# Performance work log

Hardware: AMD Instinct MI355X
Metric: run time of the kernel (lower is better)

Reference implementation:

```python
import jax, jax.numpy as jnp
import numpy as np

N_NODES = 50000
N_EDGES = 800000
IN_DIM = 256
HID_DIM = 128
N_LAYERS = 3


def setup_inputs() -> dict:
    key = jax.random.key(0)
    ks = jax.random.split(key, 7)
    s = 0.05
    x = jax.random.normal(ks[0], (N_NODES, IN_DIM), dtype=jnp.float32)
    edge_index = jax.random.randint(ks[1], (2, N_EDGES), 0, N_NODES, dtype=jnp.int64)
    W_enc = jax.random.normal(ks[2], (HID_DIM, IN_DIM), dtype=jnp.float32) * s
    b_enc = jax.random.normal(ks[3], (HID_DIM,), dtype=jnp.float32) * s
    W_l = jax.random.normal(ks[4], (N_LAYERS, HID_DIM, HID_DIM), dtype=jnp.float32) * s
    b_l = jax.random.normal(ks[5], (N_LAYERS, HID_DIM), dtype=jnp.float32) * s
    W_r = jax.random.normal(ks[6], (N_LAYERS, HID_DIM, HID_DIM), dtype=jnp.float32) * s
    return {"x": x, "edge_index": edge_index, "W_enc": W_enc, "b_enc": b_enc,
            "W_l": W_l, "b_l": b_l, "W_r": W_r}


def reference(x, edge_index, W_enc, b_enc, W_l, b_l, W_r):
    # eval mode: dropout is identity
    n = x.shape[0]
    src, dst = edge_index[0], edge_index[1]
    # encode: Linear(in_dim -> hid_dim)
    h = x @ W_enc.T + b_enc  # [N, H]
    # in-degree for mean aggregation (nodes with no in-edges -> 0 output)
    deg = jax.ops.segment_sum(jnp.ones((src.shape[0],), h.dtype), dst, num_segments=n)
    denom = jnp.maximum(deg, 1.0)[:, None]  # [N, 1]
    for i in range(W_l.shape[0]):
        # mean of source-node features over incoming edges
        agg = jax.ops.segment_sum(h[src], dst, num_segments=n) / denom  # [N, H]
        # SAGEConv: lin_l(agg) + lin_r(h)  (lin_r has no bias)
        h = agg @ W_l[i].T + b_l[i] + h @ W_r[i].T
    return h
```

## Files before the change

### kernel.cpp

```cpp
#include <hip/hip_runtime.h>

#define N_NODES 50000
#define N_EDGES 800000
#define IN_DIM 256
#define HID_DIM 128
#define ROWTILES 3125
#define ENC_BLOCKS 1024
#define WCVT_BLOCKS 48
#define CNT_BLOCKS 256
#define EDGES_PER_CB 3125
#define NBLK_LAYER 1563
#define CAP_E 352
#define TPAD 3136

typedef float f4 __attribute__((ext_vector_type(4)));
typedef float f32x4 __attribute__((ext_vector_type(4)));
typedef float vf2 __attribute__((ext_vector_type(2)));
typedef short bf16x8 __attribute__((ext_vector_type(8)));

__device__ __forceinline__ unsigned short f2bf(float f) {
    unsigned u = __builtin_bit_cast(unsigned, f);
    return (unsigned short)((u + 0x7fffu + ((u >> 16) & 1u)) >> 16);
}
__device__ __forceinline__ unsigned pk2(float a, float b) {
    return (unsigned)f2bf(a) | ((unsigned)f2bf(b) << 16);
}
__device__ __forceinline__ bf16x8 cvt8(f4 a, f4 b) {
    union { bf16x8 v; unsigned u[4]; } r;
    r.u[0] = pk2(a[0], a[1]);
    r.u[1] = pk2(a[2], a[3]);
    r.u[2] = pk2(b[0], b[1]);
    r.u[3] = pk2(b[2], b[3]);
    return r.v;
}
__device__ __forceinline__ vf2 dec8(unsigned short t) {
    return __builtin_amdgcn_cvt_pk_f32_fp8((int)(unsigned)t, false);
}
__device__ __forceinline__ void gl_lds16(const void* g, void* l) {
    __builtin_amdgcn_global_load_lds(
        (const __attribute__((address_space(1))) unsigned int*)g,
        (__attribute__((address_space(3))) unsigned int*)l, 16, 0, 0);
}


__global__ __launch_bounds__(256) void k_pre(const int* __restrict__ dst,
                                             int* __restrict__ Cm,
                                             const float* __restrict__ Wl, const float* __restrict__ Wr,
                                             unsigned short* __restrict__ wlrbf,
                                             const float* __restrict__ x,
                                             const float* __restrict__ Wenc,
                                             const float* __restrict__ bias,
                                             unsigned short* __restrict__ hout,
                                             unsigned char* __restrict__ f8out) {
    __shared__ int smem_i[8192];
    int tid = threadIdx.x;
    if (blockIdx.x < WCVT_BLOCKS) {
        int idx = blockIdx.x * 2048 + tid * 8;
        const float* srcp = (idx < 49152) ? (Wl + idx) : (Wr + (idx - 49152));
        const f4* g = (const f4*)srcp;
        *(bf16x8*)(wlrbf + idx) = cvt8(g[0], g[1]);
        return;
    }
    if (blockIdx.x >= WCVT_BLOCKS + ENC_BLOCKS) {
        int c = blockIdx.x - WCVT_BLOCKS - ENC_BLOCKS;
        int* cnt = smem_i;
        for (int i = tid; i < TPAD; i += 256) cnt[i] = 0;
        __syncthreads();
        const int* dp = dst + c * EDGES_PER_CB;
        for (int i = tid; i < EDGES_PER_CB; i += 256)
            atomicAdd(&cnt[dp[i] >> 4], 1);
        __syncthreads();
        int* crow = Cm + (size_t)c * TPAD;
        for (int t = tid; t < TPAD; t += 256) crow[t] = cnt[t];
        return;
    }
    float* xsf = (float*)smem_i;
    int bid = blockIdx.x - WCVT_BLOCKS;
    int lane = tid & 63;
    int wv = tid >> 6;
    int colbase = wv * 32;
    int lr = lane & 15;
    int kh = (lane >> 4) * 8;
    int khB = kh * 4;
    int swz = (lr & 7) << 4;

    bf16x8 bfr[2][8];
#pragma unroll
    for (int n = 0; n < 2; ++n) {
        const float* wp = Wenc + (size_t)(colbase + n * 16 + lr) * IN_DIM + kh;
#pragma unroll
        for (int s = 0; s < 8; ++s) {
            const f4* g = (const f4*)(wp + s * 32);
            bfr[n][s] = cvt8(g[0], g[1]);
        }
    }
    float bias0 = bias[colbase + lr];
    float bias1 = bias[colbase + 16 + lr];

    int pb = 0;
    for (int rt = bid; rt < ROWTILES; rt += ENC_BLOCKS, pb ^= 1) {
#pragma unroll
        for (int jj = 0; jj < 4; ++jj) {
            int j = wv * 4 + jj;
            const char* gsrc = (const char*)(x + (size_t)(rt * 16 + j) * IN_DIM)
                               + ((lane * 16) ^ ((j & 7) << 4));
            gl_lds16(gsrc, (char*)(xsf + pb * 4096) + j * 1024);
        }
        __syncthreads();

        const char* xb = (const char*)(xsf + pb * 4096) + lr * 1024;
        bf16x8 afr[8];
#pragma unroll
        for (int s = 0; s < 8; ++s) {
            int lo = khB + s * 128;
            f4 a = *(const f4*)(xb + ((lo) ^ swz));
            f4 b = *(const f4*)(xb + ((lo + 16) ^ swz));
            afr[s] = cvt8(a, b);
        }
        f32x4 acc0 = {0.f, 0.f, 0.f, 0.f}, acc1 = {0.f, 0.f, 0.f, 0.f};
#pragma unroll
        for (int s = 0; s < 8; ++s) {
            acc0 = __builtin_amdgcn_mfma_f32_16x16x32_bf16(afr[s], bfr[0][s], acc0, 0, 0, 0);
            acc1 = __builtin_amdgcn_mfma_f32_16x16x32_bf16(afr[s], bfr[1][s], acc1, 0, 0, 0);
        }
        int rbase = rt * 16 + (lane >> 4) * 4;
#pragma unroll
        for (int r = 0; r < 4; ++r) {
            float v0 = acc0[r] + bias0, v1 = acc1[r] + bias1;
            unsigned short* op = hout + (size_t)(rbase + r) * HID_DIM;
            op[colbase + lr] = f2bf(v0);
            op[colbase + 16 + lr] = f2bf(v1);
            unsigned pk = (unsigned)__builtin_amdgcn_cvt_pk_fp8_f32(v0, v1, 0, false);
            unsigned char* fp = f8out + (size_t)(rbase + r) * HID_DIM;
            fp[colbase + lr] = (unsigned char)(pk & 0xff);
            fp[colbase + 16 + lr] = (unsigned char)((pk >> 8) & 0xff);
        }
    }
}


__global__ __launch_bounds__(256) void k_prefix(const int* __restrict__ Cm,
                                                int* __restrict__ STm,
                                                int* __restrict__ tcnt16) {
    int tid = threadIdx.x;
    int lane = tid & 63;
    int t = blockIdx.x * 4 + (tid >> 6);
    if (t >= ROWTILES) return;
    int b0 = lane * 4;
    int c0 = Cm[(size_t)(b0 + 0) * TPAD + t];
    int c1 = Cm[(size_t)(b0 + 1) * TPAD + t];
    int c2 = Cm[(size_t)(b0 + 2) * TPAD + t];
    int c3 = Cm[(size_t)(b0 + 3) * TPAD + t];
    int ls = c0 + c1 + c2 + c3;
    int incl = ls;
#pragma unroll
    for (int off = 1; off < 64; off <<= 1) {
        int v = __shfl_up(incl, off);
        if (lane >= off) incl += v;
    }
    int excl = incl - ls;
    STm[(size_t)(b0 + 0) * TPAD + t] = excl;
    STm[(size_t)(b0 + 1) * TPAD + t] = excl + c0;
    STm[(size_t)(b0 + 2) * TPAD + t] = excl + c0 + c1;
    STm[(size_t)(b0 + 3) * TPAD + t] = excl + c0 + c1 + c2;
    if (lane == 63) tcnt16[t * 16] = incl;
}


__global__ __launch_bounds__(256) void k_scat(const int* __restrict__ src, const int* __restrict__ dst,
                                              const int* __restrict__ STm,
                                              unsigned* __restrict__ buf) {
    __shared__ int sbase[TPAD];
    __shared__ int lcnt[TPAD];
    int tid = threadIdx.x;
    int c = blockIdx.x;
    const int* strow = STm + (size_t)c * TPAD;
    for (int i = tid; i < TPAD; i += 256) { sbase[i] = strow[i]; lcnt[i] = 0; }
    __syncthreads();
    const int* sp = src + c * EDGES_PER_CB;
    const int* dp = dst + c * EDGES_PER_CB;
    for (int i = tid; i < EDGES_PER_CB; i += 256) {
        int sv = sp[i], dv = dp[i];
        int t = dv >> 4, dl = dv & 15;
        int r = atomicAdd(&lcnt[t], 1);
        int slot = sbase[t] + r;
        if (slot < CAP_E) buf[(size_t)t * CAP_E + slot] = (unsigned)sv | ((unsigned)dl << 16);
    }
}


__global__ __launch_bounds__(256) void k_sort2(const unsigned* __restrict__ buf,
                                               const int* __restrict__ tcnt16,
                                               unsigned short* __restrict__ idg,
                                               unsigned short* __restrict__ preft) {
    __shared__ unsigned short stmp[4][512];
    __shared__ int hcur[4][32];
    int tid = threadIdx.x, lane = tid & 63, w = tid >> 6;
    int t = blockIdx.x * 4 + w;
    bool act = t < ROWTILES;
    int cnt = 0;
    if (act) { cnt = tcnt16[t * 16]; if (cnt > CAP_E) cnt = CAP_E; }
    if (lane < 32) hcur[w][lane] = 0;
    unsigned ev[6];
#pragma unroll
    for (int k = 0; k < 6; ++k) {
        int i = lane + k * 64;
        ev[k] = (act && i < cnt) ? buf[(size_t)t * CAP_E + i] : 0xFFFFFFFFu;
    }
    __syncthreads();
#pragma unroll
    for (int k = 0; k < 6; ++k)
        if (ev[k] != 0xFFFFFFFFu) atomicAdd(&hcur[w][ev[k] >> 16], 1);
    __syncthreads();
    int hv = (lane < 16) ? hcur[w][lane] : 0;
    int incl = hv;
#pragma unroll
    for (int off = 1; off <= 16; off <<= 1) {
        int v = __shfl_up(incl, off);
        if (lane >= off) incl += v;
    }
    int excl = incl - hv;
    if (act && lane < 16) hcur[w][16 + lane] = excl;
    if (act && lane <= 16) preft[(size_t)t * 32 + lane] = (unsigned short)excl;
    __syncthreads();
#pragma unroll
    for (int k = 0; k < 6; ++k)
        if (ev[k] != 0xFFFFFFFFu) {
            int r = atomicAdd(&hcur[w][16 + (ev[k] >> 16)], 1);
            stmp[w][r] = (unsigned short)(ev[k] & 0xffff);
        }
    __syncthreads();
    if (act) {
        unsigned* op = (unsigned*)(idg + (size_t)t * 512);
        const unsigned* ip = (const unsigned*)stmp[w];
        int nu = (cnt + 1) >> 1;
        for (int i = lane; i < nu; i += 64) op[i] = ip[i];
    }
}


template <bool LAST>
__global__ __launch_bounds__(256) void k_layer(const unsigned short* __restrict__ H,
                                               const unsigned char* __restrict__ F8,
                                               const unsigned short* __restrict__ idg,
                                               const unsigned short* __restrict__ preft,
                                               const unsigned short* __restrict__ wlbf,
                                               const unsigned short* __restrict__ wrbf,
                                               const float* __restrict__ bias,
                                               unsigned short* __restrict__ hout,
                                               unsigned char* __restrict__ f8out,
                                               float* __restrict__ fout) {
    __shared__ unsigned char rowbuf[CAP_E * 128];
    __shared__ unsigned short aggs[16][136];
    __shared__ unsigned short idsb[2][512];
    int tid = threadIdx.x;
    int lane = tid & 63;
    int wv = tid >> 6;
    int colbase = wv * 32;
    int lr = lane & 15;
    int kh = (lane >> 4) * 8;

    bf16x8 bl[2][4], br[2][4];
#pragma unroll
    for (int n = 0; n < 2; ++n) {
        const unsigned short* lp = wlbf + (size_t)(colbase + n * 16 + lr) * HID_DIM + kh;
        const unsigned short* rp = wrbf + (size_t)(colbase + n * 16 + lr) * HID_DIM + kh;
#pragma unroll
        for (int s = 0; s < 4; ++s) {
            bl[n][s] = *(const bf16x8*)(lp + s * 32);
            br[n][s] = *(const bf16x8*)(rp + s * 32);
        }
    }
    float bias0 = bias[colbase + lr];
    float bias1 = bias[colbase + 16 + lr];

    int rt0 = blockIdx.x;
    gl_lds16((const char*)(idg + (size_t)rt0 * 512) + lane * 16, (void*)idsb[0]);
    int pc = (int)preft[(size_t)rt0 * 32 + (lane < 16 ? lane : 16)];
    asm volatile("s_waitcnt vmcnt(0)" ::: "memory");
    __builtin_amdgcn_sched_barrier(0);

    int pb = 0;
    for (int rt = rt0; rt < ROWTILES; rt += NBLK_LAYER, pb ^= 1) {
        int cnt = __shfl(pc, 16);
        int rb0 = __shfl(pc, wv * 4) >> 3;
        int rb1 = (__shfl(pc, wv * 4 + 4) + 7) >> 3;

        for (int i = rb0; i < rb1; ++i) {
            int ee = i * 8 + (lane >> 3);
            ee = (ee > cnt - 1) ? cnt - 1 : ee;
            const unsigned char* gp = F8 + (size_t)idsb[pb][ee] * HID_DIM + (lane & 7) * 16;
            gl_lds16(gp, &rowbuf[i * 1024]);
        }
        const unsigned short* hp = H + (size_t)(rt * 16 + lr) * HID_DIM + kh;
        bf16x8 hfr[4];
#pragma unroll
        for (int s = 0; s < 4; ++s) hfr[s] = *(const bf16x8*)(hp + s * 32);
        int rtn = rt + NBLK_LAYER;
        int pn = 0;
        if (rtn < ROWTILES) {
            gl_lds16((const char*)(idg + (size_t)rtn * 512) + lane * 16, (void*)idsb[pb ^ 1]);
            pn = (int)preft[(size_t)rtn * 32 + (lane < 16 ? lane : 16)];
        }
        asm volatile("s_waitcnt vmcnt(0)" ::: "memory");
        __builtin_amdgcn_sched_barrier(0);

#pragma unroll
        for (int q = 0; q < 4; ++q) {
            int nq = wv * 4 + q;
            int jb = __shfl(pc, nq), je = __shfl(pc, nq + 1);
            float a0 = 0.f, a1 = 0.f;
            int j = jb;
            for (; j + 4 <= je; j += 4) {
                unsigned short t0 = *(const unsigned short*)&rowbuf[(j + 0) * 128 + lane * 2];
                unsigned short t1 = *(const unsigned short*)&rowbuf[(j + 1) * 128 + lane * 2];
                unsigned short t2 = *(const unsigned short*)&rowbuf[(j + 2) * 128 + lane * 2];
                unsigned short t3 = *(const unsigned short*)&rowbuf[(j + 3) * 128 + lane * 2];
                vf2 f0 = dec8(t0), f1 = dec8(t1), f2_ = dec8(t2), f3 = dec8(t3);
                a0 += (f0[0] + f1[0]) + (f2_[0] + f3[0]);
                a1 += (f0[1] + f1[1]) + (f2_[1] + f3[1]);
            }
            for (; j < je; ++j) {
                unsigned short t0 = *(const unsigned short*)&rowbuf[j * 128 + lane * 2];
                vf2 f0 = dec8(t0);
                a0 += f0[0];
                a1 += f0[1];
            }
            int dg = je - jb;
            float inv = 1.0f / (float)(dg > 0 ? dg : 1);
            *(unsigned*)&aggs[nq][lane * 2] = pk2(a0 * inv, a1 * inv);
        }
        __syncthreads();

        bf16x8 afr[4];
#pragma unroll
        for (int s = 0; s < 4; ++s) afr[s] = *(const bf16x8*)&aggs[lr][kh + s * 32];
        f32x4 acc0 = {0.f, 0.f, 0.f, 0.f}, acc1 = {0.f, 0.f, 0.f, 0.f};
#pragma unroll
        for (int s = 0; s < 4; ++s) {
            acc0 = __builtin_amdgcn_mfma_f32_16x16x32_bf16(afr[s], bl[0][s], acc0, 0, 0, 0);
            acc1 = __builtin_amdgcn_mfma_f32_16x16x32_bf16(afr[s], bl[1][s], acc1, 0, 0, 0);
            acc0 = __builtin_amdgcn_mfma_f32_16x16x32_bf16(hfr[s], br[0][s], acc0, 0, 0, 0);
            acc1 = __builtin_amdgcn_mfma_f32_16x16x32_bf16(hfr[s], br[1][s], acc1, 0, 0, 0);
        }
        int rbase = rt * 16 + (lane >> 4) * 4;
#pragma unroll
        for (int r = 0; r < 4; ++r) {
            float v0 = acc0[r] + bias0, v1 = acc1[r] + bias1;
            if (LAST) {
                float* op = fout + (size_t)(rbase + r) * HID_DIM;
                op[colbase + lr] = v0;
                op[colbase + 16 + lr] = v1;
            } else {
                unsigned short* op = hout + (size_t)(rbase + r) * HID_DIM;
                op[colbase + lr] = f2bf(v0);
                op[colbase + 16 + lr] = f2bf(v1);
                unsigned pk = (unsigned)__builtin_amdgcn_cvt_pk_fp8_f32(v0, v1, 0, false);
                unsigned char* fp = f8out + (size_t)(rbase + r) * HID_DIM;
                fp[colbase + lr] = (unsigned char)(pk & 0xff);
                fp[colbase + 16 + lr] = (unsigned char)((pk >> 8) & 0xff);
            }
        }
        __syncthreads();
        pc = pn;
    }
}


extern "C" void kernel_launch(void* const* d_in, const int* in_sizes, int n_in,
                              void* d_out, int out_size, void* d_ws, size_t ws_size,
                              hipStream_t stream) {
    const float* x    = (const float*)d_in[0];
    const int*   ei   = (const int*)d_in[1];
    const float* Wenc = (const float*)d_in[2];
    const float* benc = (const float*)d_in[3];
    const float* Wl   = (const float*)d_in[4];
    const float* bl   = (const float*)d_in[5];
    const float* Wr   = (const float*)d_in[6];
    float* out = (float*)d_out;

    const int* srcv = ei;
    const int* dstv = ei + N_EDGES;

    char* p = (char*)d_ws;
    unsigned short* h0    = (unsigned short*)p; p += (size_t)N_NODES * HID_DIM * 2;
    unsigned short* h1    = (unsigned short*)p; p += (size_t)N_NODES * HID_DIM * 2;
    unsigned char*  h0f   = (unsigned char*)p;  p += (size_t)N_NODES * HID_DIM;
    unsigned char*  h1f   = (unsigned char*)p;  p += (size_t)N_NODES * HID_DIM;
    unsigned short* wlrbf = (unsigned short*)p; p += 98304 * 2;
    int*      tcnt16 = (int*)p;      p += 3136 * 16 * 4;
    unsigned short* idg   = (unsigned short*)p; p += (size_t)ROWTILES * 512 * 2;
    unsigned short* preft = (unsigned short*)p; p += (size_t)ROWTILES * 32 * 2;
    unsigned* buf    = (unsigned*)p; p += (size_t)ROWTILES * CAP_E * 4;

    int* Cm  = (int*)h1;
    int* STm = (int*)((char*)h1 + (size_t)CNT_BLOCKS * TPAD * 4);

    unsigned short* wlbf = wlrbf;
    unsigned short* wrbf = wlrbf + 49152;

    k_pre<<<WCVT_BLOCKS + ENC_BLOCKS + CNT_BLOCKS, 256, 0, stream>>>(
        dstv, Cm, Wl, Wr, wlrbf, x, Wenc, benc, h0, h0f);
    k_prefix<<<(ROWTILES + 3) / 4, 256, 0, stream>>>(Cm, STm, tcnt16);
    k_scat<<<CNT_BLOCKS, 256, 0, stream>>>(srcv, dstv, STm, buf);
    k_sort2<<<(ROWTILES + 3) / 4, 256, 0, stream>>>(buf, tcnt16, idg, preft);

    k_layer<false><<<NBLK_LAYER, 256, 0, stream>>>(h0, h0f, idg, preft, wlbf, wrbf, bl,
                                                   h1, h1f, nullptr);
    k_layer<false><<<NBLK_LAYER, 256, 0, stream>>>(h1, h1f, idg, preft, wlbf + 16384, wrbf + 16384,
                                                   bl + HID_DIM, h0, h0f, nullptr);
    k_layer<true><<<NBLK_LAYER, 256, 0, stream>>>(h0, h0f, idg, preft, wlbf + 32768, wrbf + 32768,
                                                  bl + 2 * HID_DIM, nullptr, nullptr, out);
}
```

Measured before the change: 179.0 us.

## Gather neighbor fp8 rows directly from global memory instead of staging through LDS

The layer kernel no longer copies every neighbor's fp8 row into a large LDS buffer with global_load_lds. Each wave now gathers neighbor rows straight from global memory, with the index lists padded to multiples of 8 that point at a zeroed dummy row, so the inner loop has no bounds checks. Blocks grow to 512 threads (8 waves, each owning 16 output columns) with weights reloaded per tile instead of held in registers, which frees LDS and registers for higher occupancy. The trade is more scattered global loads per wave and repeated weight fetches, in exchange for removing the ~45KB LDS staging and its wait.

New measurement: 364.0 us. +103.4%, slower.

```diff
diff --git a/kernel.cpp b/kernel.cpp
--- a/kernel.cpp
+++ b/kernel.cpp
@@ -9,9 +9,10 @@
 #define WCVT_BLOCKS 48
 #define CNT_BLOCKS 256
 #define EDGES_PER_CB 3125
-#define NBLK_LAYER 1563
+#define NBLK_LAYER 782
 #define CAP_E 352
 #define TPAD 3136
+#define ZID 50000
 
 typedef float f4 __attribute__((ext_vector_type(4)));
 typedef float f32x4 __attribute__((ext_vector_type(4)));
@@ -51,7 +52,8 @@
                                              const float* __restrict__ Wenc,
                                              const float* __restrict__ bias,
                                              unsigned short* __restrict__ hout,
-                                             unsigned char* __restrict__ f8out) {
+                                             unsigned char* __restrict__ f8out,
+                                             unsigned char* __restrict__ f8z2) {
     __shared__ int smem_i[8192];
     int tid = threadIdx.x;
     if (blockIdx.x < WCVT_BLOCKS) {
@@ -59,6 +61,12 @@
         const float* srcp = (idx < 49152) ? (Wl + idx) : (Wr + (idx - 49152));
         const f4* g = (const f4*)srcp;
         *(bf16x8*)(wlrbf + idx) = cvt8(g[0], g[1]);
+        if (blockIdx.x == 0 && tid >= 240) {
+            f4 z = {0.f, 0.f, 0.f, 0.f};
+            int i = tid - 240;
+            if (i < 8) *(f4*)(f8out + (size_t)ZID * HID_DIM + i * 16) = z;
+            else       *(f4*)(f8z2 + (size_t)ZID * HID_DIM + (i - 8) * 16) = z;
+        }
         return;
     }
     if (blockIdx.x >= WCVT_BLOCKS + ENC_BLOCKS) {
@@ -192,15 +200,18 @@
 __global__ __launch_bounds__(256) void k_sort2(const unsigned* __restrict__ buf,
                                                const int* __restrict__ tcnt16,
                                                unsigned short* __restrict__ idg,
-                                               unsigned short* __restrict__ preft) {
-    __shared__ unsigned short stmp[4][512];
-    __shared__ int hcur[4][32];
+                                               unsigned* __restrict__ pdat) {
+    __shared__ __align__(16) unsigned short stmp[4][512];
+    __shared__ int hc[4][32];
     int tid = threadIdx.x, lane = tid & 63, w = tid >> 6;
     int t = blockIdx.x * 4 + w;
     bool act = t < ROWTILES;
     int cnt = 0;
     if (act) { cnt = tcnt16[t * 16]; if (cnt > CAP_E) cnt = CAP_E; }
-    if (lane < 32) hcur[w][lane] = 0;
+    if (lane < 16) hc[w][lane] = 0;
+    unsigned zz = (unsigned)ZID | ((unsigned)ZID << 16);
+#pragma unroll
+    for (int i = 0; i < 4; ++i) ((unsigned*)stmp[w])[lane * 4 + i] = zz;
     unsigned ev[6];
 #pragma unroll
     for (int k = 0; k < 6; ++k) {
@@ -210,159 +221,137 @@
     __syncthreads();
 #pragma unroll
     for (int k = 0; k < 6; ++k)
-        if (ev[k] != 0xFFFFFFFFu) atomicAdd(&hcur[w][ev[k] >> 16], 1);
+        if (ev[k] != 0xFFFFFFFFu) atomicAdd(&hc[w][ev[k] >> 16], 1);
     __syncthreads();
-    int hv = (lane < 16) ? hcur[w][lane] : 0;
-    int incl = hv;
-#pragma unroll
-    for (int off = 1; off <= 16; off <<= 1) {
+    int deg = (lane < 16) ? hc[w][lane] : 0;
+    int al = (deg + 7) & ~7;
+    int incl = al;
+#pragma unroll
+    for (int off = 1; off <= 8; off <<= 1) {
         int v = __shfl_up(incl, off);
         if (lane >= off) incl += v;
     }
-    int excl = incl - hv;
-    if (act && lane < 16) hcur[w][16 + lane] = excl;
-    if (act && lane <= 16) preft[(size_t)t * 32 + lane] = (unsigned short)excl;
+    int start8 = incl - al;
+    if (act && lane < 16) {
+        hc[w][16 + lane] = start8;
+        pdat[(size_t)t * 32 + lane] = (unsigned)start8 | ((unsigned)deg << 16);
+    }
     __syncthreads();
 #pragma unroll
     for (int k = 0; k < 6; ++k)
         if (ev[k] != 0xFFFFFFFFu) {
-            int r = atomicAdd(&hcur[w][16 + (ev[k] >> 16)], 1);
+            int r = atomicAdd(&hc[w][16 + (int)(ev[k] >> 16)], 1);
             stmp[w][r] = (unsigned short)(ev[k] & 0xffff);
         }
     __syncthreads();
     if (act) {
         unsigned* op = (unsigned*)(idg + (size_t)t * 512);
         const unsigned* ip = (const unsigned*)stmp[w];
-        int nu = (cnt + 1) >> 1;
-        for (int i = lane; i < nu; i += 64) op[i] = ip[i];
+#pragma unroll
+        for (int i = 0; i < 4; ++i) op[lane * 4 + i] = ip[lane * 4 + i];
     }
 }
 
 
 template <bool LAST>
-__global__ __launch_bounds__(256) void k_layer(const unsigned short* __restrict__ H,
-                                               const unsigned char* __restrict__ F8,
-                                               const unsigned short* __restrict__ idg,
-                                               const unsigned short* __restrict__ preft,
-                                               const unsigned short* __restrict__ wlbf,
-                                               const unsigned short* __restrict__ wrbf,
-                                               const float* __restrict__ bias,
-                                               unsigned short* __restrict__ hout,
-                                               unsigned char* __restrict__ f8out,
-                                               float* __restrict__ fout) {
-    __shared__ unsigned char rowbuf[CAP_E * 128];
+__global__ __launch_bounds__(512, 8) void k_layer(const unsigned short* __restrict__ H,
+                                                  const unsigned char* __restrict__ F8,
+                                                  const unsigned short* __restrict__ idg,
+                                                  const unsigned* __restrict__ pdat,
+                                                  const unsigned short* __restrict__ wlbf,
+                                                  const unsigned short* __restrict__ wrbf,
+                                                  const float* __restrict__ bias,
+                                                  unsigned short* __restrict__ hout,
+                                                  unsigned char* __restrict__ f8out,
+                                                  float* __restrict__ fout) {
     __shared__ unsigned short aggs[16][136];
-    __shared__ unsigned short idsb[2][512];
+    __shared__ __align__(16) unsigned short idsb[2][512];
     int tid = threadIdx.x;
     int lane = tid & 63;
     int wv = tid >> 6;
-    int colbase = wv * 32;
+    int colbase = wv * 16;
     int lr = lane & 15;
     int kh = (lane >> 4) * 8;
-
-    bf16x8 bl[2][4], br[2][4];
-#pragma unroll
-    for (int n = 0; n < 2; ++n) {
-        const unsigned short* lp = wlbf + (size_t)(colbase + n * 16 + lr) * HID_DIM + kh;
-        const unsigned short* rp = wrbf + (size_t)(colbase + n * 16 + lr) * HID_DIM + kh;
-#pragma unroll
-        for (int s = 0; s < 4; ++s) {
-            bl[n][s] = *(const bf16x8*)(lp + s * 32);
-            br[n][s] = *(const bf16x8*)(rp + s * 32);
-        }
-    }
-    float bias0 = bias[colbase + lr];
-    float bias1 = bias[colbase + 16 + lr];
+    float biasv = bias[colbase + lr];
+    const unsigned short* wlp = wlbf + (size_t)(colbase + lr) * HID_DIM + kh;
+    const unsigned short* wrp = wrbf + (size_t)(colbase + lr) * HID_DIM + kh;
 
     int rt0 = blockIdx.x;
     gl_lds16((const char*)(idg + (size_t)rt0 * 512) + lane * 16, (void*)idsb[0]);
-    int pc = (int)preft[(size_t)rt0 * 32 + (lane < 16 ? lane : 16)];
-    asm volatile("s_waitcnt vmcnt(0)" ::: "memory");
-    __builtin_amdgcn_sched_barrier(0);
 
     int pb = 0;
     for (int rt = rt0; rt < ROWTILES; rt += NBLK_LAYER, pb ^= 1) {
-        int cnt = __shfl(pc, 16);
-        int rb0 = __shfl(pc, wv * 4) >> 3;
-        int rb1 = (__shfl(pc, wv * 4 + 4) + 7) >> 3;
-
-        for (int i = rb0; i < rb1; ++i) {
-            int ee = i * 8 + (lane >> 3);
-            ee = (ee > cnt - 1) ? cnt - 1 : ee;
-            const unsigned char* gp = F8 + (size_t)idsb[pb][ee] * HID_DIM + (lane & 7) * 16;
-            gl_lds16(gp, &rowbuf[i * 1024]);
-        }
-        const unsigned short* hp = H + (size_t)(rt * 16 + lr) * HID_DIM + kh;
-        bf16x8 hfr[4];
-#pragma unroll
-        for (int s = 0; s < 4; ++s) hfr[s] = *(const bf16x8*)(hp + s * 32);
-        int rtn = rt + NBLK_LAYER;
-        int pn = 0;
-        if (rtn < ROWTILES) {
-            gl_lds16((const char*)(idg + (size_t)rtn * 512) + lane * 16, (void*)idsb[pb ^ 1]);
-            pn = (int)preft[(size_t)rtn * 32 + (lane < 16 ? lane : 16)];
-        }
         asm volatile("s_waitcnt vmcnt(0)" ::: "memory");
         __builtin_amdgcn_sched_barrier(0);
-
-#pragma unroll
-        for (int q = 0; q < 4; ++q) {
-            int nq = wv * 4 + q;
-            int jb = __shfl(pc, nq), je = __shfl(pc, nq + 1);
+        unsigned pd = pdat[(size_t)rt * 32 + lr];
+
+        int rtn = rt + NBLK_LAYER;
+        if (rtn < ROWTILES)
+            gl_lds16((const char*)(idg + (size_t)rtn * 512) + lane * 16, (void*)idsb[pb ^ 1]);
+
+        const unsigned short* hp = H + (size_t)(rt * 16 + lr) * HID_DIM + kh;
+        bf16x8 xfr[4], wf[4];
+#pragma unroll
+        for (int s = 0; s < 4; ++s) {
+            xfr[s] = *(const bf16x8*)(hp + s * 32);
+            wf[s] = *(const bf16x8*)(wrp + s * 32);
+        }
+        f32x4 acc = {0.f, 0.f, 0.f, 0.f};
+#pragma unroll
+        for (int s = 0; s < 4; ++s)
+            acc = __builtin_amdgcn_mfma_f32_16x16x32_bf16(xfr[s], wf[s], acc, 0, 0, 0);
+
+#pragma unroll
+        for (int q2 = 0; q2 < 2; ++q2) {
+            int nq = wv * 2 + q2;
+            unsigned pq = __shfl(pd, nq);
+            int s8 = (int)(pq & 0xffffu);
+            int dg = (int)(pq >> 16);
+            const unsigned short* idp = &idsb[pb][s8];
             float a0 = 0.f, a1 = 0.f;
-            int j = jb;
-            for (; j + 4 <= je; j += 4) {
-                unsigned short t0 = *(const unsigned short*)&rowbuf[(j + 0) * 128 + lane * 2];
-                unsigned short t1 = *(const unsigned short*)&rowbuf[(j + 1) * 128 + lane * 2];
-                unsigned short t2 = *(const unsigned short*)&rowbuf[(j + 2) * 128 + lane * 2];
-                unsigned short t3 = *(const unsigned short*)&rowbuf[(j + 3) * 128 + lane * 2];
-                vf2 f0 = dec8(t0), f1 = dec8(t1), f2_ = dec8(t2), f3 = dec8(t3);
-                a0 += (f0[0] + f1[0]) + (f2_[0] + f3[0]);
-                a1 += (f0[1] + f1[1]) + (f2_[1] + f3[1]);
+            int nb = (dg + 7) >> 3;
+            for (int b = 0; b < nb; ++b) {
+                union { bf16x8 v; unsigned short u[8]; } iu;
+                iu.v = *(const bf16x8*)(idp + b * 8);
+                float s00 = 0.f, s01 = 0.f, s10 = 0.f, s11 = 0.f;
+#pragma unroll
+                for (int k = 0; k < 8; k += 2) {
+                    unsigned short t0 = *(const unsigned short*)(F8 + (size_t)iu.u[k] * HID_DIM + lane * 2);
+                    unsigned short t1 = *(const unsigned short*)(F8 + (size_t)iu.u[k + 1] * HID_DIM + lane * 2);
+                    vf2 f0 = dec8(t0), f1 = dec8(t1);
+                    s00 += f0[0]; s01 += f0[1];
+                    s10 += f1[0]; s11 += f1[1];
+                }
+                a0 += s00 + s10;
+                a1 += s01 + s11;
             }
-            for (; j < je; ++j) {
-                unsigned short t0 = *(const unsigned short*)&rowbuf[j * 128 + lane * 2];
-                vf2 f0 = dec8(t0);
-                a0 += f0[0];
-                a1 += f0[1];
-            }
-            int dg = je - jb;
             float inv = 1.0f / (float)(dg > 0 ? dg : 1);
             *(unsigned*)&aggs[nq][lane * 2] = pk2(a0 * inv, a1 * inv);
         }
         __syncthreads();
 
-        bf16x8 afr[4];
-#pragma unroll
-        for (int s = 0; s < 4; ++s) afr[s] = *(const bf16x8*)&aggs[lr][kh + s * 32];
-        f32x4 acc0 = {0.f, 0.f, 0.f, 0.f}, acc1 = {0.f, 0.f, 0.f, 0.f};
 #pragma unroll
         for (int s = 0; s < 4; ++s) {
-            acc0 = __builtin_amdgcn_mfma_f32_16x16x32_bf16(afr[s], bl[0][s], acc0, 0, 0, 0);
-            acc1 = __builtin_amdgcn_mfma_f32_16x16x32_bf16(afr[s], bl[1][s], acc1, 0, 0, 0);
-            acc0 = __builtin_amdgcn_mfma_f32_16x16x32_bf16(hfr[s], br[0][s], acc0, 0, 0, 0);
-            acc1 = __builtin_amdgcn_mfma_f32_16x16x32_bf16(hfr[s], br[1][s], acc1, 0, 0, 0);
-        }
+            xfr[s] = *(const bf16x8*)&aggs[lr][kh + s * 32];
+            wf[s] = *(const bf16x8*)(wlp + s * 32);
+        }
+#pragma unroll
+        for (int s = 0; s < 4; ++s)
+            acc = __builtin_amdgcn_mfma_f32_16x16x32_bf16(xfr[s], wf[s], acc, 0, 0, 0);
+
         int rbase = rt * 16 + (lane >> 4) * 4;
 #pragma unroll
         for (int r = 0; r < 4; ++r) {
-            float v0 = acc0[r] + bias0, v1 = acc1[r] + bias1;
+            float v0 = acc[r] + biasv;
             if (LAST) {
-                float* op = fout + (size_t)(rbase + r) * HID_DIM;
-                op[colbase + lr] = v0;
-                op[colbase + 16 + lr] = v1;
+                fout[(size_t)(rbase + r) * HID_DIM + colbase + lr] = v0;
             } else {
-                unsigned short* op = hout + (size_t)(rbase + r) * HID_DIM;
-                op[colbase + lr] = f2bf(v0);
-                op[colbase + 16 + lr] = f2bf(v1);
-                unsigned pk = (unsigned)__builtin_amdgcn_cvt_pk_fp8_f32(v0, v1, 0, false);
-                unsigned char* fp = f8out + (size_t)(rbase + r) * HID_DIM;
-                fp[colbase + lr] = (unsigned char)(pk & 0xff);
-                fp[colbase + 16 + lr] = (unsigned char)((pk >> 8) & 0xff);
+                hout[(size_t)(rbase + r) * HID_DIM + colbase + lr] = f2bf(v0);
+                unsigned pk = (unsigned)__builtin_amdgcn_cvt_pk_fp8_f32(v0, v0, 0, false);
+                f8out[(size_t)(rbase + r) * HID_DIM + colbase + lr] = (unsigned char)(pk & 0xff);
             }
         }
         __syncthreads();
-        pc = pn;
     }
 }
 
@@ -385,12 +374,12 @@
     char* p = (char*)d_ws;
     unsigned short* h0    = (unsigned short*)p; p += (size_t)N_NODES * HID_DIM * 2;
     unsigned short* h1    = (unsigned short*)p; p += (size_t)N_NODES * HID_DIM * 2;
-    unsigned char*  h0f   = (unsigned char*)p;  p += (size_t)N_NODES * HID_DIM;
-    unsigned char*  h1f   = (unsigned char*)p;  p += (size_t)N_NODES * HID_DIM;
+    unsigned char*  h0f   = (unsigned char*)p;  p += (size_t)N_NODES * HID_DIM + 128;
+    unsigned char*  h1f   = (unsigned char*)p;  p += (size_t)N_NODES * HID_DIM + 128;
     unsigned short* wlrbf = (unsigned short*)p; p += 98304 * 2;
     int*      tcnt16 = (int*)p;      p += 3136 * 16 * 4;
     unsigned short* idg   = (unsigned short*)p; p += (size_t)ROWTILES * 512 * 2;
-    unsigned short* preft = (unsigned short*)p; p += (size_t)ROWTILES * 32 * 2;
+    unsigned* pdat   = (unsigned*)p; p += (size_t)ROWTILES * 32 * 4;
     unsigned* buf    = (unsigned*)p; p += (size_t)ROWTILES * CAP_E * 4;
 
     int* Cm  = (int*)h1;
@@ -400,15 +389,15 @@
     unsigned short* wrbf = wlrbf + 49152;
 
     k_pre<<<WCVT_BLOCKS + ENC_BLOCKS + CNT_BLOCKS, 256, 0, stream>>>(
-        dstv, Cm, Wl, Wr, wlrbf, x, Wenc, benc, h0, h0f);
+        dstv, Cm, Wl, Wr, wlrbf, x, Wenc, benc, h0, h0f, h1f);
     k_prefix<<<(ROWTILES + 3) / 4, 256, 0, stream>>>(Cm, STm, tcnt16);
     k_scat<<<CNT_BLOCKS, 256, 0, stream>>>(srcv, dstv, STm, buf);
-    k_sort2<<<(ROWTILES + 3) / 4, 256, 0, stream>>>(buf, tcnt16, idg, preft);
-
-    k_layer<false><<<NBLK_LAYER, 256, 0, stream>>>(h0, h0f, idg, preft, wlbf, wrbf, bl,
+    k_sort2<<<(ROWTILES + 3) / 4, 256, 0, stream>>>(buf, tcnt16, idg, pdat);
+
+    k_layer<false><<<NBLK_LAYER, 512, 0, stream>>>(h0, h0f, idg, pdat, wlbf, wrbf, bl,
                                                    h1, h1f, nullptr);
-    k_layer<false><<<NBLK_LAYER, 256, 0, stream>>>(h1, h1f, idg, preft, wlbf + 16384, wrbf + 16384,
+    k_layer<false><<<NBLK_LAYER, 512, 0, stream>>>(h1, h1f, idg, pdat, wlbf + 16384, wrbf + 16384,
                                                    bl + HID_DIM, h0, h0f, nullptr);
-    k_layer<true><<<NBLK_LAYER, 256, 0, stream>>>(h0, h0f, idg, preft, wlbf + 32768, wrbf + 32768,
+    k_layer<true><<<NBLK_LAYER, 512, 0, stream>>>(h0, h0f, idg, pdat, wlbf + 32768, wrbf + 32768,
                                                   bl + 2 * HID_DIM, nullptr, nullptr, out);
 }
```

## Gather neighbor rows in two halves through a smaller LDS buffer

Applied to the files above, without the earlier changes.

Shrinks the per-block LDS row buffer from CAP_E*128 bytes to 30 KB of slots. Each wave now gathers and reduces its neighbor rows in two phases that reuse the same slots, with per-wave slot offsets computed from the prefix counts. This lowers LDS use per block so more blocks can be resident. The cost is an extra vmcnt wait per tile and less overlap, and the slot budget assumes per-tile edge counts stay small enough to fit.

Measured after the change: 189.7 us. 6.0% more time.

```diff
diff --git a/kernel.cpp b/kernel.cpp
--- a/kernel.cpp
+++ b/kernel.cpp
@@ -12,6 +12,7 @@
 #define NBLK_LAYER 1563
 #define CAP_E 352
 #define TPAD 3136
+#define RSLOTS 30
 
 typedef float f4 __attribute__((ext_vector_type(4)));
 typedef float f32x4 __attribute__((ext_vector_type(4)));
@@ -250,7 +251,7 @@
                                                unsigned short* __restrict__ hout,
                                                unsigned char* __restrict__ f8out,
                                                float* __restrict__ fout) {
-    __shared__ unsigned char rowbuf[CAP_E * 128];
+    __shared__ unsigned char rowbuf[RSLOTS * 1024];
     __shared__ unsigned short aggs[16][136];
     __shared__ unsigned short idsb[2][512];
     int tid = threadIdx.x;
@@ -283,19 +284,73 @@
     int pb = 0;
     for (int rt = rt0; rt < ROWTILES; rt += NBLK_LAYER, pb ^= 1) {
         int cnt = __shfl(pc, 16);
-        int rb0 = __shfl(pc, wv * 4) >> 3;
-        int rb1 = (__shfl(pc, wv * 4 + 4) + 7) >> 3;
-
-        for (int i = rb0; i < rb1; ++i) {
-            int ee = i * 8 + (lane >> 3);
+        int jbw = __shfl(pc, wv * 4);
+        int jew = __shfl(pc, wv * 4 + 4);
+        int rb0 = jbw >> 3;
+        int nb = ((jew + 7) >> 3) - rb0;
+        int h = (nb + 1) >> 1;
+        int p4_ = __shfl(pc, 4), p8_ = __shfl(pc, 8), p12_ = __shfl(pc, 12);
+        int nb0 = ((p4_ + 7) >> 3);
+        int nb1 = ((p8_ + 7) >> 3) - (p4_ >> 3);
+        int nb2 = ((p12_ + 7) >> 3) - (p8_ >> 3);
+        int SB = 0;
+        if (wv > 0) SB += (nb0 + 1) >> 1;
+        if (wv > 1) SB += (nb1 + 1) >> 1;
+        if (wv > 2) SB += (nb2 + 1) >> 1;
+        int wmid = (rb0 + h) * 8;
+
+        for (int gb = rb0; gb < rb0 + h; ++gb) {
+            int ee = gb * 8 + (lane >> 3);
             ee = (ee > cnt - 1) ? cnt - 1 : ee;
             const unsigned char* gp = F8 + (size_t)idsb[pb][ee] * HID_DIM + (lane & 7) * 16;
-            gl_lds16(gp, &rowbuf[i * 1024]);
+            gl_lds16(gp, &rowbuf[(SB + gb - rb0) * 1024]);
         }
         const unsigned short* hp = H + (size_t)(rt * 16 + lr) * HID_DIM + kh;
         bf16x8 hfr[4];
 #pragma unroll
         for (int s = 0; s < 4; ++s) hfr[s] = *(const bf16x8*)(hp + s * 32);
+        asm volatile("s_waitcnt vmcnt(0)" ::: "memory");
+        __builtin_amdgcn_sched_barrier(0);
+
+        float sa[4], sb_[4];
+#pragma unroll
+        for (int q = 0; q < 4; ++q) { sa[q] = 0.f; sb_[q] = 0.f; }
+
+        {
+            int off = (SB - rb0) << 10;
+#pragma unroll
+            for (int q = 0; q < 4; ++q) {
+                int jq0 = __shfl(pc, wv * 4 + q);
+                int jq1 = __shfl(pc, wv * 4 + q + 1);
+                int jhi = (jq1 < wmid) ? jq1 : wmid;
+                float a0 = 0.f, a1 = 0.f;
+                int j = jq0;
+                for (; j + 4 <= jhi; j += 4) {
+                    unsigned short t0 = *(const unsigned short*)&rowbuf[off + (j + 0) * 128 + lane * 2];
+                    unsigned short t1 = *(const unsigned short*)&rowbuf[off + (j + 1) * 128 + lane * 2];
+                    unsigned short t2 = *(const unsigned short*)&rowbuf[off + (j + 2) * 128 + lane * 2];
+                    unsigned short t3 = *(const unsigned short*)&rowbuf[off + (j + 3) * 128 + lane * 2];
+                    vf2 f0 = dec8(t0), f1 = dec8(t1), f2_ = dec8(t2), f3 = dec8(t3);
+                    a0 += (f0[0] + f1[0]) + (f2_[0] + f3[0]);
+                    a1 += (f0[1] + f1[1]) + (f2_[1] + f3[1]);
+                }
+                for (; j < jhi; ++j) {
+                    unsigned short t0 = *(const unsigned short*)&rowbuf[off + j * 128 + lane * 2];
+                    vf2 f0 = dec8(t0);
+                    a0 += f0[0];
+                    a1 += f0[1];
+                }
+                sa[q] += a0;
+                sb_[q] += a1;
+            }
+        }
+
+        for (int gb = rb0 + h; gb < rb0 + nb; ++gb) {
+            int ee = gb * 8 + (lane >> 3);
+            ee = (ee > cnt - 1) ? cnt - 1 : ee;
+            const unsigned char* gp = F8 + (size_t)idsb[pb][ee] * HID_DIM + (lane & 7) * 16;
+            gl_lds16(gp, &rowbuf[(SB + gb - rb0 - h) * 1024]);
+        }
         int rtn = rt + NBLK_LAYER;
         int pn = 0;
         if (rtn < ROWTILES) {
@@ -305,30 +360,37 @@
         asm volatile("s_waitcnt vmcnt(0)" ::: "memory");
         __builtin_amdgcn_sched_barrier(0);
 
-#pragma unroll
-        for (int q = 0; q < 4; ++q) {
-            int nq = wv * 4 + q;
-            int jb = __shfl(pc, nq), je = __shfl(pc, nq + 1);
-            float a0 = 0.f, a1 = 0.f;
-            int j = jb;
-            for (; j + 4 <= je; j += 4) {
-                unsigned short t0 = *(const unsigned short*)&rowbuf[(j + 0) * 128 + lane * 2];
-                unsigned short t1 = *(const unsigned short*)&rowbuf[(j + 1) * 128 + lane * 2];
-                unsigned short t2 = *(const unsigned short*)&rowbuf[(j + 2) * 128 + lane * 2];
-                unsigned short t3 = *(const unsigned short*)&rowbuf[(j + 3) * 128 + lane * 2];
-                vf2 f0 = dec8(t0), f1 = dec8(t1), f2_ = dec8(t2), f3 = dec8(t3);
-                a0 += (f0[0] + f1[0]) + (f2_[0] + f3[0]);
-                a1 += (f0[1] + f1[1]) + (f2_[1] + f3[1]);
+        {
+            int off = (SB - rb0 - h) << 10;
+#pragma unroll
+            for (int q = 0; q < 4; ++q) {
+                int jq0 = __shfl(pc, wv * 4 + q);
+                int jq1 = __shfl(pc, wv * 4 + q + 1);
+                int jlo = (jq0 > wmid) ? jq0 : wmid;
+                float a0 = 0.f, a1 = 0.f;
+                int j = jlo;
+                for (; j + 4 <= jq1; j += 4) {
+                    unsigned short t0 = *(const unsigned short*)&rowbuf[off + (j + 0) * 128 + lane * 2];
+                    unsigned short t1 = *(const unsigned short*)&rowbuf[off + (j + 1) * 128 + lane * 2];
+                    unsigned short t2 = *(const unsigned short*)&rowbuf[off + (j + 2) * 128 + lane * 2];
+                    unsigned short t3 = *(const unsigned short*)&rowbuf[off + (j + 3) * 128 + lane * 2];
+                    vf2 f0 = dec8(t0), f1 = dec8(t1), f2_ = dec8(t2), f3 = dec8(t3);
+                    a0 += (f0[0] + f1[0]) + (f2_[0] + f3[0]);
+                    a1 += (f0[1] + f1[1]) + (f2_[1] + f3[1]);
+                }
+                for (; j < jq1; ++j) {
+                    unsigned short t0 = *(const unsigned short*)&rowbuf[off + j * 128 + lane * 2];
+                    vf2 f0 = dec8(t0);
+                    a0 += f0[0];
+                    a1 += f0[1];
+                }
+                sa[q] += a0;
+                sb_[q] += a1;
+                int nq = wv * 4 + q;
+                int dg = jq1 - jq0;
+                float inv = 1.0f / (float)(dg > 0 ? dg : 1);
+                *(unsigned*)&aggs[nq][lane * 2] = pk2(sa[q] * inv, sb_[q] * inv);
             }
-            for (; j < je; ++j) {
-                unsigned short t0 = *(const unsigned short*)&rowbuf[j * 128 + lane * 2];
-                vf2 f0 = dec8(t0);
-                a0 += f0[0];
-                a1 += f0[1];
-            }
-            int dg = je - jb;
-            float inv = 1.0f / (float)(dg > 0 ? dg : 1);
-            *(unsigned*)&aggs[nq][lane * 2] = pk2(a0 * inv, a1 * inv);
         }
         __syncthreads();
 
```

## Gather neighbor rows directly from global memory, one tile per block

Applied to the files above, without the earlier changes.

Removes the LDS staging of gathered fp8 neighbor rows (async global-to-LDS copies plus a double-buffered index prefetch) and the persistent grid-stride loop. Each block now handles one 16-row tile and reads neighbor indices and feature bytes straight from global memory inside the accumulation loop. Dropping the ~45KB LDS buffer should allow more blocks per CU, so latency is hidden through occupancy rather than explicit prefetch. The cost is dependent index-then-row loads of only 2 bytes per lane and no cross-tile pipelining. An empty no-op loop was also added in k_sort2.

New measurement: 306.9 us. +71.5%, slower.

```diff
diff --git a/kernel.cpp b/kernel.cpp
--- a/kernel.cpp
+++ b/kernel.cpp
@@ -9,7 +9,6 @@
 #define WCVT_BLOCKS 48
 #define CNT_BLOCKS 256
 #define EDGES_PER_CB 3125
-#define NBLK_LAYER 1563
 #define CAP_E 352
 #define TPAD 3136
 
@@ -234,6 +233,7 @@
         unsigned* op = (unsigned*)(idg + (size_t)t * 512);
         const unsigned* ip = (const unsigned*)stmp[w];
         int nu = (cnt + 1) >> 1;
+        for (int i = lane; i < 64; i += 64) { }
         for (int i = lane; i < nu; i += 64) op[i] = ip[i];
     }
 }
@@ -250,15 +250,14 @@
                                                unsigned short* __restrict__ hout,
                                                unsigned char* __restrict__ f8out,
                                                float* __restrict__ fout) {
-    __shared__ unsigned char rowbuf[CAP_E * 128];
     __shared__ unsigned short aggs[16][136];
-    __shared__ unsigned short idsb[2][512];
     int tid = threadIdx.x;
     int lane = tid & 63;
     int wv = tid >> 6;
     int colbase = wv * 32;
     int lr = lane & 15;
     int kh = (lane >> 4) * 8;
+    int rt = blockIdx.x;
 
     bf16x8 bl[2][4], br[2][4];
 #pragma unroll
@@ -274,95 +273,70 @@
     float bias0 = bias[colbase + lr];
     float bias1 = bias[colbase + 16 + lr];
 
-    int rt0 = blockIdx.x;
-    gl_lds16((const char*)(idg + (size_t)rt0 * 512) + lane * 16, (void*)idsb[0]);
-    int pc = (int)preft[(size_t)rt0 * 32 + (lane < 16 ? lane : 16)];
-    asm volatile("s_waitcnt vmcnt(0)" ::: "memory");
-    __builtin_amdgcn_sched_barrier(0);
-
-    int pb = 0;
-    for (int rt = rt0; rt < ROWTILES; rt += NBLK_LAYER, pb ^= 1) {
-        int cnt = __shfl(pc, 16);
-        int rb0 = __shfl(pc, wv * 4) >> 3;
-        int rb1 = (__shfl(pc, wv * 4 + 4) + 7) >> 3;
-
-        for (int i = rb0; i < rb1; ++i) {
-            int ee = i * 8 + (lane >> 3);
-            ee = (ee > cnt - 1) ? cnt - 1 : ee;
-            const unsigned char* gp = F8 + (size_t)idsb[pb][ee] * HID_DIM + (lane & 7) * 16;
-            gl_lds16(gp, &rowbuf[i * 1024]);
-        }
-        const unsigned short* hp = H + (size_t)(rt * 16 + lr) * HID_DIM + kh;
-        bf16x8 hfr[4];
-#pragma unroll
-        for (int s = 0; s < 4; ++s) hfr[s] = *(const bf16x8*)(hp + s * 32);
-        int rtn = rt + NBLK_LAYER;
-        int pn = 0;
-        if (rtn < ROWTILES) {
-            gl_lds16((const char*)(idg + (size_t)rtn * 512) + lane * 16, (void*)idsb[pb ^ 1]);
-            pn = (int)preft[(size_t)rtn * 32 + (lane < 16 ? lane : 16)];
-        }
-        asm volatile("s_waitcnt vmcnt(0)" ::: "memory");
-        __builtin_amdgcn_sched_barrier(0);
-
-#pragma unroll
-        for (int q = 0; q < 4; ++q) {
-            int nq = wv * 4 + q;
-            int jb = __shfl(pc, nq), je = __shfl(pc, nq + 1);
-            float a0 = 0.f, a1 = 0.f;
-            int j = jb;
-            for (; j + 4 <= je; j += 4) {
-                unsigned short t0 = *(const unsigned short*)&rowbuf[(j + 0) * 128 + lane * 2];
-                unsigned short t1 = *(const unsigned short*)&rowbuf[(j + 1) * 128 + lane * 2];
-                unsigned short t2 = *(const unsigned short*)&rowbuf[(j + 2) * 128 + lane * 2];
-                unsigned short t3 = *(const unsigned short*)&rowbuf[(j + 3) * 128 + lane * 2];
-                vf2 f0 = dec8(t0), f1 = dec8(t1), f2_ = dec8(t2), f3 = dec8(t3);
-                a0 += (f0[0] + f1[0]) + (f2_[0] + f3[0]);
-                a1 += (f0[1] + f1[1]) + (f2_[1] + f3[1]);
-            }
-            for (; j < je; ++j) {
-                unsigned short t0 = *(const unsigned short*)&rowbuf[j * 128 + lane * 2];
-                vf2 f0 = dec8(t0);
-                a0 += f0[0];
-                a1 += f0[1];
-            }
-            int dg = je - jb;
-            float inv = 1.0f / (float)(dg > 0 ? dg : 1);
-            *(unsigned*)&aggs[nq][lane * 2] = pk2(a0 * inv, a1 * inv);
-        }
-        __syncthreads();
-
-        bf16x8 afr[4];
-#pragma unroll
-        for (int s = 0; s < 4; ++s) afr[s] = *(const bf16x8*)&aggs[lr][kh + s * 32];
-        f32x4 acc0 = {0.f, 0.f, 0.f, 0.f}, acc1 = {0.f, 0.f, 0.f, 0.f};
-#pragma unroll
-        for (int s = 0; s < 4; ++s) {
-            acc0 = __builtin_amdgcn_mfma_f32_16x16x32_bf16(afr[s], bl[0][s], acc0, 0, 0, 0);
-            acc1 = __builtin_amdgcn_mfma_f32_16x16x32_bf16(afr[s], bl[1][s], acc1, 0, 0, 0);
-            acc0 = __builtin_amdgcn_mfma_f32_16x16x32_bf16(hfr[s], br[0][s], acc0, 0, 0, 0);
-            acc1 = __builtin_amdgcn_mfma_f32_16x16x32_bf16(hfr[s], br[1][s], acc1, 0, 0, 0);
-        }
-        int rbase = rt * 16 + (lane >> 4) * 4;
-#pragma unroll
-        for (int r = 0; r < 4; ++r) {
-            float v0 = acc0[r] + bias0, v1 = acc1[r] + bias1;
-            if (LAST) {
-                float* op = fout + (size_t)(rbase + r) * HID_DIM;
-                op[colbase + lr] = v0;
-                op[colbase + 16 + lr] = v1;
-            } else {
-                unsigned short* op = hout + (size_t)(rbase + r) * HID_DIM;
-                op[colbase + lr] = f2bf(v0);
-                op[colbase + 16 + lr] = f2bf(v1);
-                unsigned pk = (unsigned)__builtin_amdgcn_cvt_pk_fp8_f32(v0, v1, 0, false);
-                unsigned char* fp = f8out + (size_t)(rbase + r) * HID_DIM;
-                fp[colbase + lr] = (unsigned char)(pk & 0xff);
-                fp[colbase + 16 + lr] = (unsigned char)((pk >> 8) & 0xff);
-            }
-        }
-        __syncthreads();
-        pc = pn;
+    int pc = (int)preft[(size_t)rt * 32 + (lane < 16 ? lane : 16)];
+
+    const unsigned short* hp = H + (size_t)(rt * 16 + lr) * HID_DIM + kh;
+    bf16x8 hfr[4];
+#pragma unroll
+    for (int s = 0; s < 4; ++s) hfr[s] = *(const bf16x8*)(hp + s * 32);
+
+    const unsigned short* idr = idg + (size_t)rt * 512;
+#pragma unroll
+    for (int q = 0; q < 4; ++q) {
+        int nq = wv * 4 + q;
+        int jb = __shfl(pc, nq), je = __shfl(pc, nq + 1);
+        float a0 = 0.f, a1 = 0.f;
+        int j = jb;
+        for (; j + 4 <= je; j += 4) {
+            int i0 = idr[j], i1 = idr[j + 1], i2 = idr[j + 2], i3 = idr[j + 3];
+            unsigned short t0 = *(const unsigned short*)(F8 + (size_t)i0 * HID_DIM + lane * 2);
+            unsigned short t1 = *(const unsigned short*)(F8 + (size_t)i1 * HID_DIM + lane * 2);
+            unsigned short t2 = *(const unsigned short*)(F8 + (size_t)i2 * HID_DIM + lane * 2);
+            unsigned short t3 = *(const unsigned short*)(F8 + (size_t)i3 * HID_DIM + lane * 2);
+            vf2 f0 = dec8(t0), f1 = dec8(t1), f2_ = dec8(t2), f3 = dec8(t3);
+            a0 += (f0[0] + f1[0]) + (f2_[0] + f3[0]);
+            a1 += (f0[1] + f1[1]) + (f2_[1] + f3[1]);
+        }
+        for (; j < je; ++j) {
+            unsigned short t0 = *(const unsigned short*)(F8 + (size_t)idr[j] * HID_DIM + lane * 2);
+            vf2 f0 = dec8(t0);
+            a0 += f0[0];
+            a1 += f0[1];
+        }
+        int dg = je - jb;
+        float inv = 1.0f / (float)(dg > 0 ? dg : 1);
+        *(unsigned*)&aggs[nq][lane * 2] = pk2(a0 * inv, a1 * inv);
+    }
+    __syncthreads();
+
+    bf16x8 afr[4];
+#pragma unroll
+    for (int s = 0; s < 4; ++s) afr[s] = *(const bf16x8*)&aggs[lr][kh + s * 32];
+    f32x4 acc0 = {0.f, 0.f, 0.f, 0.f}, acc1 = {0.f, 0.f, 0.f, 0.f};
+#pragma unroll
+    for (int s = 0; s < 4; ++s) {
+        acc0 = __builtin_amdgcn_mfma_f32_16x16x32_bf16(afr[s], bl[0][s], acc0, 0, 0, 0);
+        acc1 = __builtin_amdgcn_mfma_f32_16x16x32_bf16(afr[s], bl[1][s], acc1, 0, 0, 0);
+        acc0 = __builtin_amdgcn_mfma_f32_16x16x32_bf16(hfr[s], br[0][s], acc0, 0, 0, 0);
+        acc1 = __builtin_amdgcn_mfma_f32_16x16x32_bf16(hfr[s], br[1][s], acc1, 0, 0, 0);
+    }
+    int rbase = rt * 16 + (lane >> 4) * 4;
+#pragma unroll
+    for (int r = 0; r < 4; ++r) {
+        float v0 = acc0[r] + bias0, v1 = acc1[r] + bias1;
+        if (LAST) {
+            float* op = fout + (size_t)(rbase + r) * HID_DIM;
+            op[colbase + lr] = v0;
+            op[colbase + 16 + lr] = v1;
+        } else {
+            unsigned short* op = hout + (size_t)(rbase + r) * HID_DIM;
+            op[colbase + lr] = f2bf(v0);
+            op[colbase + 16 + lr] = f2bf(v1);
+            unsigned pk = (unsigned)__builtin_amdgcn_cvt_pk_fp8_f32(v0, v1, 0, false);
+            unsigned char* fp = f8out + (size_t)(rbase + r) * HID_DIM;
+            fp[colbase + lr] = (unsigned char)(pk & 0xff);
+            fp[colbase + 16 + lr] = (unsigned char)((pk >> 8) & 0xff);
+        }
     }
 }
 
@@ -405,10 +379,10 @@
     k_scat<<<CNT_BLOCKS, 256, 0, stream>>>(srcv, dstv, STm, buf);
     k_sort2<<<(ROWTILES + 3) / 4, 256, 0, stream>>>(buf, tcnt16, idg, preft);
 
-    k_layer<false><<<NBLK_LAYER, 256, 0, stream>>>(h0, h0f, idg, preft, wlbf, wrbf, bl,
-                                                   h1, h1f, nullptr);
-    k_layer<false><<<NBLK_LAYER, 256, 0, stream>>>(h1, h1f, idg, preft, wlbf + 16384, wrbf + 16384,
-                                                   bl + HID_DIM, h0, h0f, nullptr);
-    k_layer<true><<<NBLK_LAYER, 256, 0, stream>>>(h0, h0f, idg, preft, wlbf + 32768, wrbf + 32768,
-                                                  bl + 2 * HID_DIM, nullptr, nullptr, out);
-}
+    k_layer<false><<<ROWTILES, 256, 0, stream>>>(h0, h0f, idg, preft, wlbf, wrbf, bl,
+                                                 h1, h1f, nullptr);
+    k_layer<false><<<ROWTILES, 256, 0, stream>>>(h1, h1f, idg, preft, wlbf + 16384, wrbf + 16384,
+                                                 bl + HID_DIM, h0, h0f, nullptr);
+    k_layer<true><<<ROWTILES, 256, 0, stream>>>(h0, h0f, idg, preft, wlbf + 32768, wrbf + 32768,
+                                                bl + 2 * HID_DIM, nullptr, nullptr, out);
+}
```
